# Performance work log

Hardware: AMD Instinct MI355X
Metric: run time of the kernel (lower is better)

Reference implementation:

```python
import jax, jax.numpy as jnp
import numpy as np

NEG_SLOPE = 0.2


def gat_conv(x, src, dst, W, att_src, att_dst, bias, heads, out_ch, concat):
    """PyG-style GATConv (eval mode, self-loops already appended to src/dst)."""
    N = x.shape[0]
    h = (x @ W).reshape(N, heads, out_ch)                      # [N,H,C]
    a_src = jnp.einsum('nhc,hc->nh', h, att_src)               # [N,H]
    a_dst = jnp.einsum('nhc,hc->nh', h, att_dst)               # [N,H]
    e = jax.nn.leaky_relu(a_src[src] + a_dst[dst], NEG_SLOPE)  # [E,H]
    # numerically-stable softmax segmented by destination node
    emax = jax.ops.segment_max(e, dst, num_segments=N)         # [N,H]
    e = jnp.exp(e - emax[dst])
    denom = jax.ops.segment_sum(e, dst, num_segments=N)
    alpha = e / (denom[dst] + 1e-16)                           # [E,H]
    msg = h[src] * alpha[..., None]                            # [E,H,C]
    out = jax.ops.segment_sum(msg, dst, num_segments=N)        # [N,H,C]
    out = out.reshape(N, heads * out_ch) if concat else out.mean(axis=1)
    return out + bias


def setup_inputs() -> dict:
    key = jax.random.key(0)
    ks = jax.random.split(key, 9)
    N, E, IN, OUT = 100000, 1600000, 128, 40
    H1, C1 = 8, 8
    x = jax.random.normal(ks[0], (N, IN), dtype=jnp.float32)
    edge_index = jax.random.randint(ks[1], (2, E), 0, N, dtype=jnp.int64)
    s = 0.1
    return {
        'x': x,
        'edge_index': edge_index,
        'W1': jax.random.normal(ks[2], (IN, H1 * C1), dtype=jnp.float32) * s,
        'att_src1': jax.random.normal(ks[3], (H1, C1), dtype=jnp.float32) * s,
        'att_dst1': jax.random.normal(ks[4], (H1, C1), dtype=jnp.float32) * s,
        'b1': jnp.zeros((H1 * C1,), dtype=jnp.float32),
        'W2': jax.random.normal(ks[5], (H1 * C1, OUT), dtype=jnp.float32) * s,
        'att_src2': jax.random.normal(ks[6], (1, OUT), dtype=jnp.float32) * s,
        'att_dst2': jax.random.normal(ks[7], (1, OUT), dtype=jnp.float32) * s,
        'b2': jnp.zeros((OUT,), dtype=jnp.float32),
    }


def reference(x, edge_index, W1, att_src1, att_dst1, b1, W2, att_src2, att_dst2, b2):
    N = x.shape[0]
    loops = jnp.arange(N, dtype=edge_index.dtype)
    src = jnp.concatenate([edge_index[0], loops])  # self-loops (PyG default)
    dst = jnp.concatenate([edge_index[1], loops])
    h = gat_conv(x, src, dst, W1, att_src1, att_dst1, b1, 8, 8, True)
    h = jax.nn.elu(h)  # dropout is identity in eval mode
    out = gat_conv(h, src, dst, W2, att_src2, att_dst2, b2, 1, W2.shape[1], False)
    return jax.nn.log_softmax(out, axis=-1)
```

## Files before the change

### kernel.cpp

```cpp
#include <hip/hip_runtime.h>
#include <math.h>

#define NEG_SLOPE 0.2f
#define BSHIFT 8
#define MAXBUK 512

typedef __attribute__((ext_vector_type(8))) short short8;
typedef __attribute__((ext_vector_type(4))) float floatx4;

static __device__ __forceinline__ float lrelu_exp(float e) {
    e = fmaxf(e, NEG_SLOPE * e);
    return __expf(e);
}

static __device__ __forceinline__ short f2bf(float f) {
    union { float f; unsigned u; } v; v.f = f;
    unsigned r = v.u + 0x7FFFu + ((v.u >> 16) & 1u);
    return (short)(r >> 16);
}
static __device__ __forceinline__ float bf2f(unsigned short s) {
    union { float f; unsigned u; } v;
    v.u = ((unsigned)s) << 16;
    return v.f;
}
static __device__ __forceinline__ float bfpair_lo(unsigned v) {
    union { float f; unsigned u; } x; x.u = v << 16; return x.f;
}
static __device__ __forceinline__ float bfpair_hi(unsigned v) {
    union { float f; unsigned u; } x; x.u = v & 0xffff0000u; return x.f;
}
static __device__ __forceinline__ void splitbf(float f, short& hi, short& lo) {
    hi = f2bf(f);
    lo = f2bf(f - bf2f((unsigned short)hi));
}


__global__ __launch_bounds__(512) void k_hist_prep(const int* __restrict__ dst, int E, int CHUNK,
                                                   int NBLK, int NBUK,
                                                   int* __restrict__ blockhist,
                                                   const float* __restrict__ W1,
                                                   short* __restrict__ w1t,
                                                   const float* __restrict__ W2,
                                                   short* __restrict__ w2ht,
                                                   short* __restrict__ w2lt) {
    __shared__ int hist[MAXBUK];
    int t = threadIdx.x, b = blockIdx.x;
    if (b < NBLK) {
        for (int i = t; i < NBUK; i += 512) hist[i] = 0;
        __syncthreads();
        int e0 = b * CHUNK, e1 = e0 + CHUNK; if (e1 > E) e1 = E;
        for (int e = e0 + t; e < e1; e += 512) atomicAdd(&hist[dst[e] >> BSHIFT], 1);
        __syncthreads();
        for (int i = t; i < NBUK; i += 512) blockhist[(size_t)i * NBLK + b] = hist[i];
    } else {
        int i = (b - NBLK) * 512 + t;
        if (i < 64 * 128) {
            int n = i >> 7, k = i & 127;
            w1t[i] = f2bf(W1[k * 64 + n]);
        } else if (i < 64 * 128 + 48 * 64) {
            int j = i - 64 * 128;
            int n = j >> 6, k = j & 63;
            short hi = 0, lo = 0;
            if (n < 40) splitbf(W2[k * 40 + n], hi, lo);
            w2ht[j] = hi; w2lt[j] = lo;
        }
    }
}

__global__ __launch_bounds__(256) void k_colscan(int* __restrict__ blockhist,
                                                 int* __restrict__ btot, int NBLK) {
    int bucket = blockIdx.x, t = threadIdx.x;
    int lane = t & 63, wv = t >> 6;
    __shared__ int wsum[4];
    __shared__ int carry_s;
    if (t == 0) carry_s = 0;
    __syncthreads();
    for (int base = 0; base < NBLK; base += 256) {
        int idx = base + t;
        int v = (idx < NBLK) ? blockhist[(size_t)bucket * NBLK + idx] : 0;
        int s = v;
#pragma unroll
        for (int o = 1; o < 64; o <<= 1) {
            int u = __shfl_up(s, o, 64);
            if (lane >= o) s += u;
        }
        if (lane == 63) wsum[wv] = s;
        __syncthreads();
        int b0 = 0;
#pragma unroll
        for (int w = 0; w < 4; ++w) b0 += (w < wv) ? wsum[w] : 0;
        int excl = s + b0 - v + carry_s;
        if (idx < NBLK) blockhist[(size_t)bucket * NBLK + idx] = excl;
        __syncthreads();
        if (t == 255) carry_s += s + b0;
        __syncthreads();
    }
    if (t == 0) btot[bucket] = carry_s;
}

__global__ __launch_bounds__(512) void k_bucket_scan(const int* __restrict__ btot,
                                                     int* __restrict__ bucketbase, int NBUK) {
    __shared__ int sh[512];
    int t = threadIdx.x;
    int v = (t < NBUK) ? btot[t] : 0;
    sh[t] = v;
    __syncthreads();
#pragma unroll
    for (int o = 1; o < 512; o <<= 1) {
        int u = (t >= o) ? sh[t - o] : 0;
        __syncthreads();
        sh[t] += u;
        __syncthreads();
    }
    if (t < NBUK) bucketbase[t] = sh[t] - v;
    if (t == NBUK - 1) bucketbase[NBUK] = sh[t];
}

__global__ __launch_bounds__(512) void k_part_gemm1(const int* __restrict__ src,
                                                    const int* __restrict__ dst, int E, int CHUNK,
                                                    int NBLK, int NBUK,
                                                    const int* __restrict__ blockhist,
                                                    const int* __restrict__ bucketbase,
                                                    unsigned* __restrict__ packed,
                                                    const float* __restrict__ x,
                                                    const short* __restrict__ w1t,
                                                    const float* __restrict__ att_s,
                                                    const float* __restrict__ att_d,
                                                    unsigned short* __restrict__ h1b,
                                                    float* __restrict__ a_s1,
                                                    float* __restrict__ a_d1, int N) {
    __shared__ int cur[MAXBUK];
    int t = threadIdx.x, b = blockIdx.x;
    if (b < NBLK) {
        for (int i = t; i < NBUK; i += 512)
            cur[i] = blockhist[(size_t)i * NBLK + b] + bucketbase[i];
        __syncthreads();
        int e0 = b * CHUNK, e1 = e0 + CHUNK; if (e1 > E) e1 = E;
        for (int e = e0 + t; e < e1; e += 512) {
            int d = dst[e], s = src[e];
            int pos = atomicAdd(&cur[d >> BSHIFT], 1);
            packed[pos] = ((unsigned)s << 8) | ((unsigned)d & 255u);
        }
        return;
    }
    int wave = t >> 6, lane = t & 63;
    int n16 = lane & 15, q = lane >> 4;
    int nb = (b - NBLK) * 128 + wave * 16;
    if (nb >= N) return;

    short8 bfr[4][4];
#pragma unroll
    for (int ct = 0; ct < 4; ++ct) {
        int n = ct * 16 + n16;
#pragma unroll
        for (int kc = 0; kc < 4; ++kc)
            bfr[ct][kc] = *(const short8*)(w1t + n * 128 + kc * 32 + q * 8);
    }

    int arow = nb + n16; if (arow >= N) arow = N - 1;
    const float* xr = x + (size_t)arow * 128 + q * 8;
    short8 afr[4];
#pragma unroll
    for (int kc = 0; kc < 4; ++kc) {
        float4 u0 = *(const float4*)(xr + kc * 32);
        float4 u1 = *(const float4*)(xr + kc * 32 + 4);
        short8 a;
        a[0] = f2bf(u0.x); a[1] = f2bf(u0.y); a[2] = f2bf(u0.z); a[3] = f2bf(u0.w);
        a[4] = f2bf(u1.x); a[5] = f2bf(u1.y); a[6] = f2bf(u1.z); a[7] = f2bf(u1.w);
        afr[kc] = a;
    }

    floatx4 acc[4];
#pragma unroll
    for (int ct = 0; ct < 4; ++ct) {
        floatx4 c = {0.f, 0.f, 0.f, 0.f};
#pragma unroll
        for (int kc = 0; kc < 4; ++kc)
            c = __builtin_amdgcn_mfma_f32_16x16x32_bf16(afr[kc], bfr[ct][kc], c, 0, 0, 0);
        acc[ct] = c;
    }

#pragma unroll
    for (int ct = 0; ct < 4; ++ct) {
#pragma unroll
        for (int r = 0; r < 4; ++r) {
            int row = nb + q * 4 + r;
            if (row < N) h1b[(size_t)row * 64 + ct * 16 + n16] = (unsigned short)f2bf(acc[ct][r]);
        }
    }

#pragma unroll
    for (int ct = 0; ct < 4; ++ct) {
        float as = att_s[ct * 16 + n16];
        float ad = att_d[ct * 16 + n16];
#pragma unroll
        for (int r = 0; r < 4; ++r) {
            float ps = acc[ct][r] * as;
            float pd = acc[ct][r] * ad;
#pragma unroll
            for (int m = 1; m < 8; m <<= 1) {
                ps += __shfl_xor(ps, m, 64);
                pd += __shfl_xor(pd, m, 64);
            }
            int row = nb + q * 4 + r;
            if ((n16 & 7) == 0 && row < N) {
                int h = 2 * ct + (n16 >> 3);
                a_s1[row * 8 + h] = ps;
                a_d1[row * 8 + h] = pd;
            }
        }
    }
}

__global__ __launch_bounds__(256) void k_fine(const unsigned* __restrict__ packed,
                                              const int* __restrict__ bucketbase,
                                              int* __restrict__ offsets,
                                              int* __restrict__ csr_src,
                                              int N, int NBUK) {
    __shared__ int fcnt[256];
    __shared__ int wsum[4];
    int bucket = blockIdx.x, t = threadIdx.x;
    int lo = bucket << BSHIFT;
    int nn = N - lo; if (nn > 256) nn = 256;
    int ebase = bucketbase[bucket];
    int ecnt = bucketbase[bucket + 1] - ebase;
    fcnt[t] = 0;
    __syncthreads();
    for (int i = t; i < ecnt; i += 256) {
        unsigned p = packed[ebase + i];
        atomicAdd(&fcnt[p & 255u], 1);
    }
    __syncthreads();
    int v = fcnt[t];
    int lane = t & 63, wv = t >> 6;
    int s = v;
#pragma unroll
    for (int o = 1; o < 64; o <<= 1) {
        int u = __shfl_up(s, o, 64);
        if (lane >= o) s += u;
    }
    if (lane == 63) wsum[wv] = s;
    __syncthreads();
    int base = 0;
#pragma unroll
    for (int w = 0; w < 4; ++w) base += (w < wv) ? wsum[w] : 0;
    int excl = s + base - v;
    if (t < nn) offsets[lo + t] = ebase + excl;
    if (bucket == NBUK - 1 && t == 0) offsets[N] = ebase + ecnt;
    __syncthreads();
    fcnt[t] = excl;
    __syncthreads();
    for (int i = t; i < ecnt; i += 256) {
        unsigned p = packed[ebase + i];
        int pos = atomicAdd(&fcnt[p & 255u], 1);
        csr_src[ebase + pos] = (int)(p >> 8);
    }
}

__global__ __launch_bounds__(256) void k_agg1(const unsigned short* __restrict__ h1b,
                                              const float* __restrict__ a_s1,
                                              const float* __restrict__ a_d1,
                                              const int* __restrict__ offsets,
                                              const int* __restrict__ csr_src,
                                              const float* __restrict__ b1,
                                              float* __restrict__ y1, int N) {
    int wave = threadIdx.x >> 6, lane = threadIdx.x & 63;
    int q = lane >> 4;
    int ll = lane & 15;
    int d = (blockIdx.x * 4 + wave) * 4 + q;
    bool dvalid = (d < N);
    int de = dvalid ? d : N - 1;
    int g = ll >> 3;
    int c = ll & 7;
    float ad = a_d1[de * 8 + c];
    int i0 = offsets[de];
    int deg = dvalid ? (offsets[de + 1] - i0) : 0;
    int dmax = deg;
    dmax = max(dmax, __shfl_xor(dmax, 16, 64));
    dmax = max(dmax, __shfl_xor(dmax, 32, 64));
    float acc[8] = {0.f, 0.f, 0.f, 0.f, 0.f, 0.f, 0.f, 0.f};
    float wsum_l = 0.f;
    if (g == 0) {
        float w0 = lrelu_exp(a_s1[de * 8 + c] + ad);
        uint4 v = *(const uint4*)(h1b + (size_t)de * 64 + 8 * c);
        acc[0] = w0 * bfpair_lo(v.x); acc[1] = w0 * bfpair_hi(v.x);
        acc[2] = w0 * bfpair_lo(v.y); acc[3] = w0 * bfpair_hi(v.y);
        acc[4] = w0 * bfpair_lo(v.z); acc[5] = w0 * bfpair_hi(v.z);
        acc[6] = w0 * bfpair_lo(v.w); acc[7] = w0 * bfpair_hi(v.w);
        wsum_l = w0;
    }
    for (int j = 0; j < dmax; j += 8) {
        int b0 = i0 + j + 4 * g;
        int idx[4]; bool lv[4];
#pragma unroll
        for (int u = 0; u < 4; ++u) {
            int jj = j + 4 * g + u;
            lv[u] = (jj < deg);
            idx[u] = de;
            if (lv[u]) idx[u] = csr_src[b0 + u];
        }
        float ev[4];
#pragma unroll
        for (int u = 0; u < 4; ++u) ev[u] = a_s1[idx[u] * 8 + c] + ad;
        uint4 vv[4];
#pragma unroll
        for (int u = 0; u < 4; ++u)
            vv[u] = *(const uint4*)(h1b + (size_t)idx[u] * 64 + 8 * c);
#pragma unroll
        for (int u = 0; u < 4; ++u) {
            float w = lv[u] ? lrelu_exp(ev[u]) : 0.f;
            wsum_l += w;
            acc[0] = fmaf(w, bfpair_lo(vv[u].x), acc[0]);
            acc[1] = fmaf(w, bfpair_hi(vv[u].x), acc[1]);
            acc[2] = fmaf(w, bfpair_lo(vv[u].y), acc[2]);
            acc[3] = fmaf(w, bfpair_hi(vv[u].y), acc[3]);
            acc[4] = fmaf(w, bfpair_lo(vv[u].z), acc[4]);
            acc[5] = fmaf(w, bfpair_hi(vv[u].z), acc[5]);
            acc[6] = fmaf(w, bfpair_lo(vv[u].w), acc[6]);
            acc[7] = fmaf(w, bfpair_hi(vv[u].w), acc[7]);
        }
    }
#pragma unroll
    for (int k = 0; k < 8; ++k) acc[k] += __shfl(acc[k], lane + 8, 64);
    wsum_l += __shfl(wsum_l, lane + 8, 64);
    if (g == 0 && dvalid) {
        float inv = 1.f / (wsum_l + 1e-16f);
        float4 bA = *(const float4*)(b1 + 8 * c);
        float4 bB = *(const float4*)(b1 + 8 * c + 4);
        float o[8];
        o[0] = acc[0] * inv + bA.x;
        o[1] = acc[1] * inv + bA.y;
        o[2] = acc[2] * inv + bA.z;
        o[3] = acc[3] * inv + bA.w;
        o[4] = acc[4] * inv + bB.x;
        o[5] = acc[5] * inv + bB.y;
        o[6] = acc[6] * inv + bB.z;
        o[7] = acc[7] * inv + bB.w;
#pragma unroll
        for (int k = 0; k < 8; ++k) o[k] = o[k] > 0.f ? o[k] : (__expf(o[k]) - 1.f);
        float4 s0 = make_float4(o[0], o[1], o[2], o[3]);
        float4 s1 = make_float4(o[4], o[5], o[6], o[7]);
        *(float4*)(y1 + (size_t)d * 64 + 8 * c) = s0;
        *(float4*)(y1 + (size_t)d * 64 + 8 * c + 4) = s1;
    }
}

__global__ __launch_bounds__(256) void k_gemm2(const float* __restrict__ y1,
                                               const short* __restrict__ w2ht,
                                               const short* __restrict__ w2lt,
                                               const float* __restrict__ att_s,
                                               const float* __restrict__ att_d,
                                               unsigned short* __restrict__ h2b,
                                               float* __restrict__ a2s,
                                               float* __restrict__ a2d, int N) {
    int tid = threadIdx.x, wave = tid >> 6, lane = tid & 63;
    int n16 = lane & 15, q = lane >> 4;
    int nb = blockIdx.x * 64 + wave * 16;
    if (nb >= N) return;

    int arow = nb + n16; if (arow >= N) arow = N - 1;
    const float* yr = y1 + (size_t)arow * 64 + q * 8;
    short8 ah[2], al[2];
#pragma unroll
    for (int kc = 0; kc < 2; ++kc) {
        float4 u0 = *(const float4*)(yr + kc * 32);
        float4 u1 = *(const float4*)(yr + kc * 32 + 4);
        short8 h, l; short hi, lo;
        splitbf(u0.x, hi, lo); h[0] = hi; l[0] = lo;
        splitbf(u0.y, hi, lo); h[1] = hi; l[1] = lo;
        splitbf(u0.z, hi, lo); h[2] = hi; l[2] = lo;
        splitbf(u0.w, hi, lo); h[3] = hi; l[3] = lo;
        splitbf(u1.x, hi, lo); h[4] = hi; l[4] = lo;
        splitbf(u1.y, hi, lo); h[5] = hi; l[5] = lo;
        splitbf(u1.z, hi, lo); h[6] = hi; l[6] = lo;
        splitbf(u1.w, hi, lo); h[7] = hi; l[7] = lo;
        ah[kc] = h; al[kc] = l;
    }

    float psr[4] = {0.f, 0.f, 0.f, 0.f}, pdr[4] = {0.f, 0.f, 0.f, 0.f};
#pragma unroll
    for (int ct = 0; ct < 3; ++ct) {
        int n = ct * 16 + n16;
        short8 bh0 = *(const short8*)(w2ht + n * 64 + q * 8);
        short8 bh1 = *(const short8*)(w2ht + n * 64 + 32 + q * 8);
        short8 bl0 = *(const short8*)(w2lt + n * 64 + q * 8);
        short8 bl1 = *(const short8*)(w2lt + n * 64 + 32 + q * 8);
        floatx4 c = {0.f, 0.f, 0.f, 0.f};
        c = __builtin_amdgcn_mfma_f32_16x16x32_bf16(ah[0], bl0, c, 0, 0, 0);
        c = __builtin_amdgcn_mfma_f32_16x16x32_bf16(al[0], bh0, c, 0, 0, 0);
        c = __builtin_amdgcn_mfma_f32_16x16x32_bf16(ah[0], bh0, c, 0, 0, 0);
        c = __builtin_amdgcn_mfma_f32_16x16x32_bf16(ah[1], bl1, c, 0, 0, 0);
        c = __builtin_amdgcn_mfma_f32_16x16x32_bf16(al[1], bh1, c, 0, 0, 0);
        c = __builtin_amdgcn_mfma_f32_16x16x32_bf16(ah[1], bh1, c, 0, 0, 0);

        int col = ct * 16 + n16;
#pragma unroll
        for (int r = 0; r < 4; ++r) {
            int row = nb + q * 4 + r;
            if (col < 40 && row < N) h2b[(size_t)row * 48 + col] = (unsigned short)f2bf(c[r]);
        }
        float asv = (col < 40) ? att_s[col] : 0.f;
        float adv = (col < 40) ? att_d[col] : 0.f;
#pragma unroll
        for (int r = 0; r < 4; ++r) {
            psr[r] = fmaf(c[r], asv, psr[r]);
            pdr[r] = fmaf(c[r], adv, pdr[r]);
        }
    }
#pragma unroll
    for (int r = 0; r < 4; ++r) {
        float ps = psr[r], pd = pdr[r];
#pragma unroll
        for (int m = 1; m < 16; m <<= 1) {
            ps += __shfl_xor(ps, m, 64);
            pd += __shfl_xor(pd, m, 64);
        }
        int row = nb + q * 4 + r;
        if (n16 == 0 && row < N) { a2s[row] = ps; a2d[row] = pd; }
    }
}

__global__ __launch_bounds__(256) void k_agg2(const unsigned short* __restrict__ h2b,
                                              const float* __restrict__ a2s,
                                              const float* __restrict__ a2d,
                                              const int* __restrict__ offsets,
                                              const int* __restrict__ csr_src,
                                              const float* __restrict__ b2,
                                              float* __restrict__ out, int N) {
    int wave = threadIdx.x >> 6, lane = threadIdx.x & 63;
    int q = lane >> 4;
    int ll = lane & 15;
    int d = (blockIdx.x * 4 + wave) * 4 + q;
    bool dvalid = (d < N);
    int de = dvalid ? d : N - 1;
    int g = ll / 5;
    int c = ll - g * 5;
    bool lane_ok = (ll < 15);
    float ad = a2d[de];
    float w0 = lrelu_exp(a2s[de] + ad);
    int i0 = offsets[de];
    int deg = offsets[de + 1] - i0;
    if (!dvalid) deg = 0;
    int dmax = deg;
    dmax = max(dmax, __shfl_xor(dmax, 16, 64));
    dmax = max(dmax, __shfl_xor(dmax, 32, 64));
    float acc[8] = {0.f, 0.f, 0.f, 0.f, 0.f, 0.f, 0.f, 0.f};
    float wsum_l = 0.f;
    if (g == 0) {
        uint4 v = *(const uint4*)(h2b + (size_t)de * 48 + 8 * c);
        acc[0] = w0 * bfpair_lo(v.x); acc[1] = w0 * bfpair_hi(v.x);
        acc[2] = w0 * bfpair_lo(v.y); acc[3] = w0 * bfpair_hi(v.y);
        acc[4] = w0 * bfpair_lo(v.z); acc[5] = w0 * bfpair_hi(v.z);
        acc[6] = w0 * bfpair_lo(v.w); acc[7] = w0 * bfpair_hi(v.w);
    }
    for (int j = 0; j < dmax; j += 12) {
        int b0 = i0 + j + 4 * g;
        int idx[4]; bool lv[4];
#pragma unroll
        for (int u = 0; u < 4; ++u) {
            int jj = j + 4 * g + u;
            lv[u] = lane_ok && (jj < deg);
            idx[u] = de;
            if (lv[u]) idx[u] = csr_src[b0 + u];
        }
        float ev[4];
#pragma unroll
        for (int u = 0; u < 4; ++u) ev[u] = a2s[idx[u]] + ad;
        uint4 vv[4];
#pragma unroll
        for (int u = 0; u < 4; ++u)
            vv[u] = *(const uint4*)(h2b + (size_t)idx[u] * 48 + 8 * c);
#pragma unroll
        for (int u = 0; u < 4; ++u) {
            float w = lv[u] ? lrelu_exp(ev[u]) : 0.f;
            if (c == 0) wsum_l += w;
            acc[0] = fmaf(w, bfpair_lo(vv[u].x), acc[0]);
            acc[1] = fmaf(w, bfpair_hi(vv[u].x), acc[1]);
            acc[2] = fmaf(w, bfpair_lo(vv[u].y), acc[2]);
            acc[3] = fmaf(w, bfpair_hi(vv[u].y), acc[3]);
            acc[4] = fmaf(w, bfpair_lo(vv[u].z), acc[4]);
            acc[5] = fmaf(w, bfpair_hi(vv[u].z), acc[5]);
            acc[6] = fmaf(w, bfpair_lo(vv[u].w), acc[6]);
            acc[7] = fmaf(w, bfpair_hi(vv[u].w), acc[7]);
        }
    }
#pragma unroll
    for (int k = 0; k < 8; ++k)
        acc[k] += __shfl(acc[k], lane + 5, 64) + __shfl(acc[k], lane + 10, 64);
    wsum_l += __shfl(wsum_l, lane + 5, 64) + __shfl(wsum_l, lane + 10, 64);
    wsum_l = __shfl(wsum_l, lane & 48, 64);
    float wsum = wsum_l + w0;
    bool act5 = (ll < 5) && dvalid;
    float inv = 1.f / (wsum + 1e-16f);
    float4 bA = *(const float4*)(b2 + 8 * c);
    float4 bB = *(const float4*)(b2 + 8 * c + 4);
    float o[8];
    o[0] = acc[0] * inv + bA.x;
    o[1] = acc[1] * inv + bA.y;
    o[2] = acc[2] * inv + bA.z;
    o[3] = acc[3] * inv + bA.w;
    o[4] = acc[4] * inv + bB.x;
    o[5] = acc[5] * inv + bB.y;
    o[6] = acc[6] * inv + bB.z;
    o[7] = acc[7] * inv + bB.w;
    float mxl = -INFINITY;
    if (act5) {
        mxl = fmaxf(fmaxf(fmaxf(o[0], o[1]), fmaxf(o[2], o[3])),
                    fmaxf(fmaxf(o[4], o[5]), fmaxf(o[6], o[7])));
    }
#pragma unroll
    for (int mm = 1; mm < 8; mm <<= 1) mxl = fmaxf(mxl, __shfl_xor(mxl, mm, 64));
    float exl = 0.f;
    if (act5) {
#pragma unroll
        for (int k = 0; k < 8; ++k) exl += __expf(o[k] - mxl);
    }
#pragma unroll
    for (int mm = 1; mm < 8; mm <<= 1) exl += __shfl_xor(exl, mm, 64);
    if (act5) {
        float lse = mxl + __logf(exl);
        float4 s0 = make_float4(o[0] - lse, o[1] - lse, o[2] - lse, o[3] - lse);
        float4 s1 = make_float4(o[4] - lse, o[5] - lse, o[6] - lse, o[7] - lse);
        *(float4*)(out + (size_t)d * 40 + 8 * c) = s0;
        *(float4*)(out + (size_t)d * 40 + 8 * c + 4) = s1;
    }
}


extern "C" void kernel_launch(void* const* d_in, const int* in_sizes, int n_in,
                              void* d_out, int out_size, void* d_ws, size_t ws_size,
                              hipStream_t stream) {
    const float* x   = (const float*)d_in[0];
    const int*   ei  = (const int*)d_in[1];
    const float* W1  = (const float*)d_in[2];
    const float* as1 = (const float*)d_in[3];
    const float* ad1 = (const float*)d_in[4];
    const float* b1  = (const float*)d_in[5];
    const float* W2  = (const float*)d_in[6];
    const float* as2 = (const float*)d_in[7];
    const float* ad2 = (const float*)d_in[8];
    const float* b2  = (const float*)d_in[9];
    float* out = (float*)d_out;

    int N = in_sizes[0] / 128;
    int E = in_sizes[1] / 2;
    const int* src = ei;
    const int* dst = ei + E;

    int NBUK = (N + 255) >> BSHIFT;
    int CHUNK = 4096;
    int NBLK = (E + CHUNK - 1) / CHUNK;

    char* ws = (char*)d_ws;
    size_t off = 0;
    auto alloc = [&](size_t bytes) -> char* {
        char* p = ws + off;
        off += (bytes + 255) & ~(size_t)255;
        return p;
    };
    unsigned short* h1b = (unsigned short*)alloc((size_t)N * 64 * 2);
    float* a_s1    = (float*)alloc((size_t)N * 8 * 4);
    float* a_d1    = (float*)alloc((size_t)N * 8 * 4);
    float* y1      = (float*)alloc((size_t)N * 64 * 4);
    size_t shared_sz = (size_t)N * 48 * 2;
    if ((size_t)E * 4 > shared_sz) shared_sz = (size_t)E * 4;
    char*  region  = alloc(shared_sz);
    unsigned short* h2b = (unsigned short*)region;
    unsigned* packed    = (unsigned*)region;
    float* a2s     = (float*)alloc((size_t)N * 4);
    float* a2d     = (float*)alloc((size_t)N * 4);
    int*   offsets = (int*)alloc((size_t)(N + 1) * 4);
    int*   csr_src = (int*)alloc((size_t)E * 4);
    int*   blockhist  = (int*)alloc((size_t)NBUK * NBLK * 4);
    int*   btot       = (int*)alloc((size_t)NBUK * 4);
    int*   bucketbase = (int*)alloc((size_t)(NBUK + 1) * 4);
    short* w1t     = (short*)alloc((size_t)64 * 128 * 2);
    short* w2ht    = (short*)alloc((size_t)48 * 64 * 2);
    short* w2lt    = (short*)alloc((size_t)48 * 64 * 2);

    int nb1 = (N + 15) / 16;
    int nb2 = (N + 15) / 16;
    int gb2 = (N + 63) / 64;
    int GB1 = (N + 127) / 128;
    int PREPB = 22;

    k_hist_prep<<<NBLK + PREPB, 512, 0, stream>>>(dst, E, CHUNK, NBLK, NBUK, blockhist,
                                                  W1, w1t, W2, w2ht, w2lt);
    k_colscan<<<NBUK, 256, 0, stream>>>(blockhist, btot, NBLK);
    k_bucket_scan<<<1, 512, 0, stream>>>(btot, bucketbase, NBUK);
    k_part_gemm1<<<NBLK + GB1, 512, 0, stream>>>(src, dst, E, CHUNK, NBLK, NBUK, blockhist,
                                                 bucketbase, packed,
                                                 x, w1t, as1, ad1, h1b, a_s1, a_d1, N);
    k_fine<<<NBUK, 256, 0, stream>>>(packed, bucketbase, offsets, csr_src, N, NBUK);
    k_agg1<<<nb1, 256, 0, stream>>>(h1b, a_s1, a_d1, offsets, csr_src, b1, y1, N);
    k_gemm2<<<gb2, 256, 0, stream>>>(y1, w2ht, w2lt, as2, ad2, h2b, a2s, a2d, N);
    k_agg2<<<nb2, 256, 0, stream>>>(h2b, a2s, a2d, offsets, csr_src, b2, out, N);
}
```

Measured before the change: 171.4 us.

## Move GEMM1 into histogram kernel and stage W1 conversion in shared memory

GEMM1 blocks now run in the same launch as the destination histogram instead of alongside the partition scatter, so the dense work overlaps the histogram phase. Each GEMM1 block converts W1 to bf16 into padded shared memory itself, which removes the global w1t buffer and its separate prep step. Partition becomes a standalone kernel. The cost is that every GEMM block re-reads and converts the whole W1 (32KB) and uses extra LDS, which may lower occupancy.

```diff
diff --git a/kernel.cpp b/kernel.cpp
--- a/kernel.cpp
+++ b/kernel.cpp
@@ -35,117 +35,50 @@
 }
 
 
-__global__ __launch_bounds__(512) void k_hist_prep(const int* __restrict__ dst, int E, int CHUNK,
-                                                   int NBLK, int NBUK,
-                                                   int* __restrict__ blockhist,
-                                                   const float* __restrict__ W1,
-                                                   short* __restrict__ w1t,
-                                                   const float* __restrict__ W2,
-                                                   short* __restrict__ w2ht,
-                                                   short* __restrict__ w2lt) {
-    __shared__ int hist[MAXBUK];
-    int t = threadIdx.x, b = blockIdx.x;
-    if (b < NBLK) {
-        for (int i = t; i < NBUK; i += 512) hist[i] = 0;
-        __syncthreads();
-        int e0 = b * CHUNK, e1 = e0 + CHUNK; if (e1 > E) e1 = E;
-        for (int e = e0 + t; e < e1; e += 512) atomicAdd(&hist[dst[e] >> BSHIFT], 1);
-        __syncthreads();
-        for (int i = t; i < NBUK; i += 512) blockhist[(size_t)i * NBLK + b] = hist[i];
-    } else {
-        int i = (b - NBLK) * 512 + t;
-        if (i < 64 * 128) {
-            int n = i >> 7, k = i & 127;
-            w1t[i] = f2bf(W1[k * 64 + n]);
-        } else if (i < 64 * 128 + 48 * 64) {
-            int j = i - 64 * 128;
-            int n = j >> 6, k = j & 63;
-            short hi = 0, lo = 0;
-            if (n < 40) splitbf(W2[k * 40 + n], hi, lo);
-            w2ht[j] = hi; w2lt[j] = lo;
-        }
-    }
-}
-
-__global__ __launch_bounds__(256) void k_colscan(int* __restrict__ blockhist,
-                                                 int* __restrict__ btot, int NBLK) {
-    int bucket = blockIdx.x, t = threadIdx.x;
-    int lane = t & 63, wv = t >> 6;
-    __shared__ int wsum[4];
-    __shared__ int carry_s;
-    if (t == 0) carry_s = 0;
-    __syncthreads();
-    for (int base = 0; base < NBLK; base += 256) {
-        int idx = base + t;
-        int v = (idx < NBLK) ? blockhist[(size_t)bucket * NBLK + idx] : 0;
-        int s = v;
-#pragma unroll
-        for (int o = 1; o < 64; o <<= 1) {
-            int u = __shfl_up(s, o, 64);
-            if (lane >= o) s += u;
-        }
-        if (lane == 63) wsum[wv] = s;
-        __syncthreads();
-        int b0 = 0;
-#pragma unroll
-        for (int w = 0; w < 4; ++w) b0 += (w < wv) ? wsum[w] : 0;
-        int excl = s + b0 - v + carry_s;
-        if (idx < NBLK) blockhist[(size_t)bucket * NBLK + idx] = excl;
-        __syncthreads();
-        if (t == 255) carry_s += s + b0;
-        __syncthreads();
-    }
-    if (t == 0) btot[bucket] = carry_s;
-}
-
-__global__ __launch_bounds__(512) void k_bucket_scan(const int* __restrict__ btot,
-                                                     int* __restrict__ bucketbase, int NBUK) {
-    __shared__ int sh[512];
-    int t = threadIdx.x;
-    int v = (t < NBUK) ? btot[t] : 0;
-    sh[t] = v;
-    __syncthreads();
-#pragma unroll
-    for (int o = 1; o < 512; o <<= 1) {
-        int u = (t >= o) ? sh[t - o] : 0;
-        __syncthreads();
-        sh[t] += u;
-        __syncthreads();
-    }
-    if (t < NBUK) bucketbase[t] = sh[t] - v;
-    if (t == NBUK - 1) bucketbase[NBUK] = sh[t];
-}
-
-__global__ __launch_bounds__(512) void k_part_gemm1(const int* __restrict__ src,
-                                                    const int* __restrict__ dst, int E, int CHUNK,
-                                                    int NBLK, int NBUK,
-                                                    const int* __restrict__ blockhist,
-                                                    const int* __restrict__ bucketbase,
-                                                    unsigned* __restrict__ packed,
+__global__ __launch_bounds__(512) void k_hist_gemm1(const int* __restrict__ dst, int E,
+                                                    int CHUNK, int NBLK, int NBUK,
+                                                    int* __restrict__ blockhist,
+                                                    const float* __restrict__ W2,
+                                                    short* __restrict__ w2ht,
+                                                    short* __restrict__ w2lt,
                                                     const float* __restrict__ x,
-                                                    const short* __restrict__ w1t,
+                                                    const float* __restrict__ W1,
                                                     const float* __restrict__ att_s,
                                                     const float* __restrict__ att_d,
                                                     unsigned short* __restrict__ h1b,
                                                     float* __restrict__ a_s1,
                                                     float* __restrict__ a_d1, int N) {
-    __shared__ int cur[MAXBUK];
+    __shared__ int hist[MAXBUK];
+    __shared__ short w1s[64 * 136];
     int t = threadIdx.x, b = blockIdx.x;
     if (b < NBLK) {
-        for (int i = t; i < NBUK; i += 512)
-            cur[i] = blockhist[(size_t)i * NBLK + b] + bucketbase[i];
+        for (int i = t; i < NBUK; i += 512) hist[i] = 0;
         __syncthreads();
         int e0 = b * CHUNK, e1 = e0 + CHUNK; if (e1 > E) e1 = E;
-        for (int e = e0 + t; e < e1; e += 512) {
-            int d = dst[e], s = src[e];
-            int pos = atomicAdd(&cur[d >> BSHIFT], 1);
-            packed[pos] = ((unsigned)s << 8) | ((unsigned)d & 255u);
-        }
+        for (int e = e0 + t; e < e1; e += 512) atomicAdd(&hist[dst[e] >> BSHIFT], 1);
+        __syncthreads();
+        for (int i = t; i < NBUK; i += 512) blockhist[(size_t)i * NBLK + b] = hist[i];
         return;
     }
+    if (b < NBLK + 6) {
+        int j = (b - NBLK) * 512 + t;
+        if (j < 48 * 64) {
+            int n = j >> 6, k = j & 63;
+            short hi = 0, lo = 0;
+            if (n < 40) splitbf(W2[k * 40 + n], hi, lo);
+            w2ht[j] = hi; w2lt[j] = lo;
+        }
+        return;
+    }
+    int gb = b - NBLK - 6;
+    for (int i = t; i < 64 * 128; i += 512) {
+        int k = i >> 6, n = i & 63;
+        w1s[n * 136 + k] = f2bf(W1[i]);
+    }
+    __syncthreads();
     int wave = t >> 6, lane = t & 63;
     int n16 = lane & 15, q = lane >> 4;
-    int nb = (b - NBLK) * 128 + wave * 16;
+    int nb = gb * 128 + wave * 16;
     if (nb >= N) return;
 
     short8 bfr[4][4];
@@ -154,7 +87,7 @@
         int n = ct * 16 + n16;
 #pragma unroll
         for (int kc = 0; kc < 4; ++kc)
-            bfr[ct][kc] = *(const short8*)(w1t + n * 128 + kc * 32 + q * 8);
+            bfr[ct][kc] = *(const short8*)(w1s + n * 136 + kc * 32 + q * 8);
     }
 
     int arow = nb + n16; if (arow >= N) arow = N - 1;
@@ -209,6 +142,74 @@
                 a_d1[row * 8 + h] = pd;
             }
         }
+    }
+}
+
+__global__ __launch_bounds__(256) void k_colscan(int* __restrict__ blockhist,
+                                                 int* __restrict__ btot, int NBLK) {
+    int bucket = blockIdx.x, t = threadIdx.x;
+    int lane = t & 63, wv = t >> 6;
+    __shared__ int wsum[4];
+    __shared__ int carry_s;
+    if (t == 0) carry_s = 0;
+    __syncthreads();
+    for (int base = 0; base < NBLK; base += 256) {
+        int idx = base + t;
+        int v = (idx < NBLK) ? blockhist[(size_t)bucket * NBLK + idx] : 0;
+        int s = v;
+#pragma unroll
+        for (int o = 1; o < 64; o <<= 1) {
+            int u = __shfl_up(s, o, 64);
+            if (lane >= o) s += u;
+        }
+        if (lane == 63) wsum[wv] = s;
+        __syncthreads();
+        int b0 = 0;
+#pragma unroll
+        for (int w = 0; w < 4; ++w) b0 += (w < wv) ? wsum[w] : 0;
+        int excl = s + b0 - v + carry_s;
+        if (idx < NBLK) blockhist[(size_t)bucket * NBLK + idx] = excl;
+        __syncthreads();
+        if (t == 255) carry_s += s + b0;
+        __syncthreads();
+    }
+    if (t == 0) btot[bucket] = carry_s;
+}
+
+__global__ __launch_bounds__(512) void k_bucket_scan(const int* __restrict__ btot,
+                                                     int* __restrict__ bucketbase, int NBUK) {
+    __shared__ int sh[512];
+    int t = threadIdx.x;
+    int v = (t < NBUK) ? btot[t] : 0;
+    sh[t] = v;
+    __syncthreads();
+#pragma unroll
+    for (int o = 1; o < 512; o <<= 1) {
+        int u = (t >= o) ? sh[t - o] : 0;
+        __syncthreads();
+        sh[t] += u;
+        __syncthreads();
+    }
+    if (t < NBUK) bucketbase[t] = sh[t] - v;
+    if (t == NBUK - 1) bucketbase[NBUK] = sh[t];
+}
+
+__global__ __launch_bounds__(512) void k_partition(const int* __restrict__ src,
+                                                   const int* __restrict__ dst, int E, int CHUNK,
+                                                   int NBLK, int NBUK,
+                                                   const int* __restrict__ blockhist,
+                                                   const int* __restrict__ bucketbase,
+                                                   unsigned* __restrict__ packed) {
+    __shared__ int cur[MAXBUK];
+    int t = threadIdx.x, b = blockIdx.x;
+    for (int i = t; i < NBUK; i += 512)
+        cur[i] = blockhist[(size_t)i * NBLK + b] + bucketbase[i];
+    __syncthreads();
+    int e0 = b * CHUNK, e1 = e0 + CHUNK; if (e1 > E) e1 = E;
+    for (int e = e0 + t; e < e1; e += 512) {
+        int d = dst[e], s = src[e];
+        int pos = atomicAdd(&cur[d >> BSHIFT], 1);
+        packed[pos] = ((unsigned)s << 8) | ((unsigned)d & 255u);
     }
 }
 
@@ -574,7 +575,6 @@
     int*   blockhist  = (int*)alloc((size_t)NBUK * NBLK * 4);
     int*   btot       = (int*)alloc((size_t)NBUK * 4);
     int*   bucketbase = (int*)alloc((size_t)(NBUK + 1) * 4);
-    short* w1t     = (short*)alloc((size_t)64 * 128 * 2);
     short* w2ht    = (short*)alloc((size_t)48 * 64 * 2);
     short* w2lt    = (short*)alloc((size_t)48 * 64 * 2);
 
@@ -582,15 +582,15 @@
     int nb2 = (N + 15) / 16;
     int gb2 = (N + 63) / 64;
     int GB1 = (N + 127) / 128;
-    int PREPB = 22;
-
-    k_hist_prep<<<NBLK + PREPB, 512, 0, stream>>>(dst, E, CHUNK, NBLK, NBUK, blockhist,
-                                                  W1, w1t, W2, w2ht, w2lt);
+    int W2B = 6;
+
+    k_hist_gemm1<<<NBLK + W2B + GB1, 512, 0, stream>>>(dst, E, CHUNK, NBLK, NBUK, blockhist,
+                                                       W2, w2ht, w2lt,
+                                                       x, W1, as1, ad1, h1b, a_s1, a_d1, N);
     k_colscan<<<NBUK, 256, 0, stream>>>(blockhist, btot, NBLK);
     k_bucket_scan<<<1, 512, 0, stream>>>(btot, bucketbase, NBUK);
-    k_part_gemm1<<<NBLK + GB1, 512, 0, stream>>>(src, dst, E, CHUNK, NBLK, NBUK, blockhist,
-                                                 bucketbase, packed,
-                                                 x, w1t, as1, ad1, h1b, a_s1, a_d1, N);
+    k_partition<<<NBLK, 512, 0, stream>>>(src, dst, E, CHUNK, NBLK, NBUK, blockhist,
+                                          bucketbase, packed);
     k_fine<<<NBUK, 256, 0, stream>>>(packed, bucketbase, offsets, csr_src, N, NBUK);
     k_agg1<<<nb1, 256, 0, stream>>>(h1b, a_s1, a_d1, offsets, csr_src, b1, y1, N);
     k_gemm2<<<gb2, 256, 0, stream>>>(y1, w2ht, w2lt, as2, ad2, h2b, a2s, a2d, N);
```

Result: faster. 165.9 us (-3.2%).
